# Performance work log

Hardware: AMD Instinct MI355X
Metric: run time of the kernel (lower is better)

Reference implementation:

```python
import jax, jax.numpy as jnp
import numpy as np

N = 16384; E = 131072; H = 128; RBF = 64; L = 4; NH = 8; HD = 16; SP = 100
CU = 10.0
ALPHA = 5.0 / CU
_start = float(np.exp(-CU))
MEANS = jnp.asarray(np.linspace(_start, 1.0, RBF, dtype=np.float32))
BETA = float(((2.0 / RBF) * (1.0 - _start)) ** -2)


def cutoff_fn(d):
    # cosine cutoff, cutoff_lower=0, cutoff_upper=CU
    return 0.5 * (jnp.cos(d * (np.pi / CU)) + 1.0) * (d < CU)


def expnorm_rbf(d):
    # d: (E,) -> (E, RBF)  exp-normal smearing (trainable=False)
    return cutoff_fn(d)[:, None] * jnp.exp(-BETA * (jnp.exp(-ALPHA * d)[:, None] - MEANS) ** 2)


def layernorm(x, g, b, eps=1e-6):
    m = x.mean(-1, keepdims=True)
    v = ((x - m) ** 2).mean(-1, keepdims=True)
    return (x - m) / jnp.sqrt(v + eps) * g + b


def setup_inputs() -> dict:
    key = jax.random.key(0)
    ks = jax.random.split(key, 20)
    def w(k, shape, fan):
        return jax.random.normal(k, shape, jnp.float32) / np.sqrt(fan)
    inp = {}
    inp["atomic_number"] = jax.random.randint(ks[0], (N,), 0, SP)
    inp["position"] = jax.random.normal(ks[1], (N, 3), jnp.float32) * 3.0
    inp["senders"] = jax.random.randint(ks[2], (E,), 0, N)
    inp["receivers"] = jax.random.randint(ks[3], (E,), 0, N)
    inp["embed1"] = w(ks[4], (SP, H), 1.0)
    inp["embed2"] = w(ks[5], (SP, H), 1.0)
    inp["nb_Wdist"] = w(ks[6], (RBF, H), RBF); inp["nb_bdist"] = jnp.zeros((H,), jnp.float32)
    inp["nb_Wcomb"] = w(ks[7], (2 * H, H), 2 * H); inp["nb_bcomb"] = jnp.zeros((H,), jnp.float32)
    inp["ln_g"] = jnp.ones((L, H), jnp.float32); inp["ln_b"] = jnp.zeros((L, H), jnp.float32)
    inp["Wq"] = w(ks[8], (L, H, H), H); inp["bq"] = jnp.zeros((L, H), jnp.float32)
    inp["Wk"] = w(ks[9], (L, H, H), H); inp["bk"] = jnp.zeros((L, H), jnp.float32)
    inp["Wv"] = w(ks[10], (L, H, 3 * H), H); inp["bv"] = jnp.zeros((L, 3 * H), jnp.float32)
    inp["Wvec"] = w(ks[11], (L, H, 3 * H), H)
    inp["Wdk"] = w(ks[12], (L, RBF, H), RBF); inp["bdk"] = jnp.zeros((L, H), jnp.float32)
    inp["Wdv"] = w(ks[13], (L, RBF, 3 * H), RBF); inp["bdv"] = jnp.zeros((L, 3 * H), jnp.float32)
    inp["Wo"] = w(ks[14], (L, H, 3 * H), H); inp["bo"] = jnp.zeros((L, 3 * H), jnp.float32)
    inp["coors_scale"] = jnp.full((L,), 0.01, jnp.float32)
    inp["lnf_g"] = jnp.ones((H,), jnp.float32); inp["lnf_b"] = jnp.zeros((H,), jnp.float32)
    return inp


def reference(atomic_number, position, senders, receivers, embed1, embed2,
              nb_Wdist, nb_bdist, nb_Wcomb, nb_bcomb, ln_g, ln_b,
              Wq, bq, Wk, bk, Wv, bv, Wvec, Wdk, bdk, Wdv, bdv, Wo, bo,
              coors_scale, lnf_g, lnf_b):
    eps = 1e-6
    n = atomic_number.shape[0]
    x = embed1[atomic_number]                               # (N,H)
    edge_vec = position[receivers] - position[senders]      # (E,3)
    edge_weight = jnp.linalg.norm(edge_vec + eps, axis=-1)  # (E,)
    edge_attr = expnorm_rbf(edge_weight)                    # (E,RBF)
    self_mask = senders == receivers
    mew = (edge_weight * (~self_mask) + self_mask)[:, None]
    mew = jnp.clip(mew, 0.01)                               # clip_during_norm
    edge_vec = edge_vec / mew                               # unit edge directions
    C = cutoff_fn(edge_weight[:, None])                     # (E,1)

    # Neighbor embedding
    Wmsg = (edge_attr @ nb_Wdist + nb_bdist) * C            # (E,H)
    msg = embed2[atomic_number[senders]] * Wmsg
    x_nb = jax.ops.segment_sum(msg, receivers, num_segments=n)
    x = jnp.concatenate([x, x_nb], axis=-1) @ nb_Wcomb + nb_bcomb

    vec = jnp.zeros((n, 3, H), x.dtype)
    for l in range(L):
        xn = layernorm(x, ln_g[l], ln_b[l])
        q = (xn @ Wq[l] + bq[l]).reshape(n, NH, HD)
        k = (xn @ Wk[l] + bk[l]).reshape(n, NH, HD)
        v = (xn @ Wv[l] + bv[l]).reshape(n, NH, 3 * HD)
        # qk_norm: l2-normalize per head
        q = q / (jnp.linalg.norm(q, axis=-1, keepdims=True) + eps)
        k = k / (jnp.linalg.norm(k, axis=-1, keepdims=True) + eps)
        # norm_coors (CoorsNorm with learned scale)
        vnorm = jnp.sqrt(jnp.clip((vec ** 2).sum(axis=1, keepdims=True), 1e-8))
        vn = vec / vnorm * coors_scale[l]
        vp = jnp.einsum('nvc,cd->nvd', vn, Wvec[l])          # (N,3,3H)
        vec1, vec2, vec3 = jnp.split(vp, 3, axis=-1)
        vec_dot = (vec1 * vec2).sum(axis=1)                  # (N,H)
        dk = jax.nn.silu(edge_attr @ Wdk[l] + bdk[l]).reshape(-1, NH, HD)
        dv = jax.nn.silu(edge_attr @ Wdv[l] + bdv[l]).reshape(-1, NH, 3 * HD)
        attn = (q[receivers] * k[senders] * dk).sum(-1)      # (E,NH)
        attn = jax.nn.silu(attn) * C                         # cutoff-weighted
        vj = v[senders] * dv                                 # (E,NH,3HD)
        xh, s1, s2 = jnp.split(vj, 3, axis=-1)
        xh = (xh * attn[..., None]).reshape(-1, H)
        s1 = s1.reshape(-1, H); s2 = s2.reshape(-1, H)
        vec_j = vec[senders] * s1[:, None, :] + s2[:, None, :] * edge_vec[:, :, None]
        x_agg = jax.ops.segment_sum(xh, receivers, num_segments=n)
        vec_agg = jax.ops.segment_sum(vec_j, receivers, num_segments=n)
        o = x_agg @ Wo[l] + bo[l]
        o1, o2, o3 = jnp.split(o, 3, axis=-1)
        x = x + vec_dot * o2 + o3
        vec = vec + vec3 * o1[:, None, :] + vec_agg
    x = layernorm(x, lnf_g, lnf_b)
    return (x, vec)
```

## Files before the change

### kernel.cpp

```cpp
#include <hip/hip_runtime.h>
#include <math.h>

#define NN 16384
#define NE 131072
#define HDIM 128
#define NRBF 64
#define NL 4

typedef __attribute__((ext_vector_type(8))) short short8;
typedef __attribute__((ext_vector_type(4))) float f32x4;
typedef __attribute__((ext_vector_type(2))) float f32x2;

__device__ __forceinline__ float siluf(float x){ return x / (1.0f + expf(-x)); }
__device__ __forceinline__ float cutofff(float d){
  return (d < 10.0f) ? 0.5f*(cosf(d*0.31415926535897932f)+1.0f) : 0.0f;
}
__device__ __forceinline__ unsigned short f2bf(float f){
  union{float f; unsigned u;} v; v.f = f;
  unsigned r = v.u + 0x7FFF + ((v.u>>16)&1);
  return (unsigned short)(r>>16);
}
__device__ __forceinline__ float bf2f(unsigned short b){
  union{unsigned u; float f;} v; v.u = ((unsigned)b)<<16;
  return v.f;
}
__device__ __forceinline__ float bflo(unsigned u){
  union{unsigned x; float f;} v; v.x = u<<16; return v.f;
}
__device__ __forceinline__ float bfhi(unsigned u){
  union{unsigned x; float f;} v; v.x = u & 0xffff0000u; return v.f;
}

__global__ void k_edge_geom(const float* __restrict__ pos, const int* __restrict__ snd,
                            const int* __restrict__ rcv, float* __restrict__ ew,
                            float* __restrict__ evec){
  int e = blockIdx.x*blockDim.x + threadIdx.x;
  if(e >= NE) return;
  int s = snd[e], r = rcv[e];
  float dx = pos[r*3+0]-pos[s*3+0];
  float dy = pos[r*3+1]-pos[s*3+1];
  float dz = pos[r*3+2]-pos[s*3+2];
  const float eps = 1e-6f;
  float d = sqrtf((dx+eps)*(dx+eps)+(dy+eps)*(dy+eps)+(dz+eps)*(dz+eps));
  ew[e] = d;
  float mew = (s==r) ? 1.0f : d;
  mew = fmaxf(mew, 0.01f);
  float inv = 1.0f/mew;
  evec[e*3+0]=dx*inv; evec[e*3+1]=dy*inv; evec[e*3+2]=dz*inv;
}

__global__ void k_hist(const int* __restrict__ rcv, int* __restrict__ deg){
  int e = blockIdx.x*256+threadIdx.x;
  if(e<NE) atomicAdd(&deg[rcv[e]],1);
}
__global__ __launch_bounds__(1024) void k_scan(const int* __restrict__ deg,
                                               int* __restrict__ off, int* __restrict__ cursor){
  __shared__ int part[1024];
  int t=threadIdx.x;
  int loc[16]; int s=0;
  #pragma unroll
  for(int i=0;i<16;i++){ loc[i]=s; s+=deg[t*16+i]; }
  part[t]=s; __syncthreads();
  for(int d=1;d<1024;d<<=1){
    int v=(t>=d)?part[t-d]:0; __syncthreads(); part[t]+=v; __syncthreads();
  }
  int excl = (t>0)?part[t-1]:0;
  #pragma unroll
  for(int i=0;i<16;i++){ int o=excl+loc[i]; off[t*16+i]=o; cursor[t*16+i]=o; }
  if(t==1023) off[NN]=part[1023];
}
__global__ void k_scatter(const int* __restrict__ rcv, int* __restrict__ cursor,
                          int* __restrict__ eidx){
  int e = blockIdx.x*256+threadIdx.x; if(e>=NE) return;
  int p = atomicAdd(&cursor[rcv[e]],1);
  eidx[p]=e;
}
__global__ void k_permute(const int* __restrict__ eidx, const float* __restrict__ ew,
                          const float* __restrict__ evec, const int* __restrict__ snd,
                          const int* __restrict__ rcv,
                          float* __restrict__ ews, float* __restrict__ cw,
                          float* __restrict__ evs, int* __restrict__ snds,
                          int* __restrict__ rcvs){
  int i = blockIdx.x*256+threadIdx.x; if(i>=NE) return;
  int e = eidx[i];
  float d = ew[e];
  ews[i]=d; cw[i]=cutofff(d);
  evs[i*3+0]=evec[e*3+0]; evs[i*3+1]=evec[e*3+1]; evs[i*3+2]=evec[e*3+2];
  snds[i]=snd[e]; rcvs[i]=rcv[e];
}

__global__ void k_cvt_nbT(const float* __restrict__ Wd, unsigned short* __restrict__ dst){
  int o = blockIdx.x*256+threadIdx.x; if(o>=HDIM*NRBF) return;
  int n=o>>6, k=o&63;
  dst[o] = f2bf(Wd[k*HDIM+n]);
}
__global__ void k_cvt_qkvT(const float* __restrict__ Wq, const float* __restrict__ Wk,
                           const float* __restrict__ Wv, unsigned short* __restrict__ dst){
  int o = blockIdx.x*256+threadIdx.x;
  if(o >= 4*640*128) return;
  int l = o/81920; int rem = o - l*81920;
  int n = rem>>7, k = rem&127;
  float v;
  if(n<128)      v = Wq[(size_t)l*16384 + k*128 + n];
  else if(n<256) v = Wk[(size_t)l*16384 + k*128 + (n-128)];
  else           v = Wv[(size_t)l*49152 + k*384 + (n-256)];
  dst[o]=f2bf(v);
}
__global__ void k_cvtT(const float* __restrict__ src, unsigned short* __restrict__ dst, int NC){
  int o = blockIdx.x*256+threadIdx.x;
  int tot = 4*NC*128; if(o>=tot) return;
  int l = o/(NC*128); int rem = o - l*NC*128;
  int n = rem>>7, k = rem&127;
  dst[o] = f2bf(src[(size_t)l*128*NC + k*NC + n]);
}
__global__ void k_wcvt4(const float* __restrict__ Wdk, const float* __restrict__ Wdv,
                        unsigned short* __restrict__ wbT4){
  int o = blockIdx.x*blockDim.x + threadIdx.x;
  if(o >= 4*512*64) return;
  int l = o >> 15; int rem = o & 32767;
  int n = rem >> 6, kk = rem & 63;
  float v = (n < 128) ? Wdk[(size_t)l*NRBF*HDIM + kk*HDIM + n]
                      : Wdv[(size_t)l*NRBF*384 + kk*384 + (n-128)];
  wbT4[o] = f2bf(v);
}
__global__ void k_bcvt4(const float* __restrict__ bdk, const float* __restrict__ bdv,
                        float* __restrict__ bias4){
  int o = threadIdx.x + blockIdx.x*blockDim.x;
  if(o >= 4*512) return;
  int l = o >> 9, c = o & 511;
  bias4[o] = (c < 128) ? bdk[l*HDIM + c] : bdv[l*384 + (c-128)];
}

__global__ __launch_bounds__(256) void k_nb_gemm(const float* __restrict__ ews,
    const float* __restrict__ cw, const int* __restrict__ snds,
    const int* __restrict__ z, const float* __restrict__ embed2,
    const unsigned short* __restrict__ nbT, const float* __restrict__ bd,
    unsigned short* __restrict__ msgc){
  __shared__ __align__(16) unsigned short Bl[HDIM*64];
  int t = threadIdx.x;
  int e0 = blockIdx.x*64;
  #pragma unroll
  for(int i=0;i<4;i++){
    int idx=i*256+t; int n=idx>>3, kc=idx&7;
    short8 val = *(const short8*)(nbT + n*64 + kc*8);
    *(short8*)((char*)Bl + n*128 + ((kc ^ (n&7))<<4)) = val;
  }
  int w=t>>6, l=t&63, lr=l&15, lg=l>>4;
  float d = ews[e0 + w*16 + lr];
  short8 a0, a1;
  {
    float edm = expf(-0.5f*d);
    float Cc = cutofff(d);
    const float start = expf(-10.0f);
    const float tmp = (2.0f/64.0f)*(1.0f-start);
    const float beta = 1.0f/(tmp*tmp);
    #pragma unroll
    for(int si=0;si<8;si++){
      float m0 = start + (1.0f-start)*((float)(lg*8+si)*(1.0f/63.0f));
      float m1 = start + (1.0f-start)*((float)(32+lg*8+si)*(1.0f/63.0f));
      float t0 = edm-m0, t1 = edm-m1;
      a0[si] = (short)f2bf(Cc*expf(-beta*t0*t0));
      a1[si] = (short)f2bf(Cc*expf(-beta*t1*t1));
    }
  }
  int sr[4]; float Cr[4]; int zz[4];
  #pragma unroll
  for(int r=0;r<4;r++){
    int i = e0 + w*16 + lg*4 + r;
    sr[r]=snds[i]; Cr[r]=cw[i]; zz[r]=z[sr[r]];
  }
  __syncthreads();
  #pragma unroll
  for(int nt=0;nt<8;nt++){
    int n=nt*16+lr;
    const char* bp=(const char*)Bl + n*128;
    short8 b0 = *(const short8*)(bp + (((lg  )^(n&7))<<4));
    short8 b1 = *(const short8*)(bp + (((4+lg)^(n&7))<<4));
    f32x4 acc={0.f,0.f,0.f,0.f};
    acc = __builtin_amdgcn_mfma_f32_16x16x32_bf16(a0,b0,acc,0,0,0);
    acc = __builtin_amdgcn_mfma_f32_16x16x32_bf16(a1,b1,acc,0,0,0);
    float bdn = bd[n];
    #pragma unroll
    for(int r=0;r<4;r++){
      float m = (acc[r]+bdn)*Cr[r]*embed2[(size_t)zz[r]*HDIM+n];
      msgc[(size_t)(e0+w*16+lg*4+r)*HDIM + n] = f2bf(m);
    }
  }
}
__global__ void k_nb_sweep(const int* __restrict__ off,
                           const unsigned short* __restrict__ msgc,
                           float* __restrict__ xnb){
  int j = threadIdx.x;
  int n0 = blockIdx.x*8;
  for(int nn=0;nn<8;nn++){
    int node=n0+nn;
    float acc=0.f;
    int ib=off[node], ie=off[node+1];
    for(int i=ib;i<ie;i++) acc += bf2f(msgc[(size_t)i*HDIM+j]);
    xnb[(size_t)node*HDIM+j]=acc;
  }
}

__global__ __launch_bounds__(256) void k_combine_b(
    const int* __restrict__ z, const float* __restrict__ embed1,
    const float* __restrict__ xnb, const float* __restrict__ Wc,
    const float* __restrict__ bc, float* __restrict__ x){
  __shared__ float sx[16][2*HDIM];
  int t = threadIdx.x; int n0 = blockIdx.x*16;
  #pragma unroll
  for(int i=0;i<16;i++){
    int idx = i*256+t; int nn = idx>>8, c = idx&255;
    int n = n0+nn;
    sx[nn][c] = (c<128) ? embed1[(size_t)z[n]*HDIM + c]
                        : xnb[(size_t)n*HDIM + (c-128)];
  }
  __syncthreads();
  int j = t&127, g = t>>7;
  float bcj = bc[j];
  float acc[8];
  #pragma unroll
  for(int r=0;r<8;r++) acc[r]=bcj;
  for(int i=0;i<2*HDIM;i++){
    float wv = Wc[i*HDIM+j];
    #pragma unroll
    for(int r=0;r<8;r++) acc[r] += sx[2*r+g][i]*wv;
  }
  #pragma unroll
  for(int r=0;r<8;r++) x[(size_t)(n0+2*r+g)*HDIM+j] = acc[r];
}

#define PADR 136
__global__ __launch_bounds__(256) void k_node_pre_m(
    const float* __restrict__ x, const float* __restrict__ vec,
    const float* __restrict__ lng, const float* __restrict__ lnb,
    const float* __restrict__ bq, const float* __restrict__ bk,
    const float* __restrict__ bv, const unsigned short* __restrict__ WqkvT,
    const unsigned short* __restrict__ WvecT, const float* __restrict__ cscale,
    unsigned short* __restrict__ qbf, unsigned short* __restrict__ kbf,
    unsigned short* __restrict__ vbf, float* __restrict__ vdot,
    float* __restrict__ vec3, int l){
  __shared__ unsigned short sxn[32][PADR];
  __shared__ unsigned short svn[3][32][PADR];
  int t = threadIdx.x, w = t>>6, lane = t&63;
  int n0 = blockIdx.x*32;
  float cs = cscale[l];
  float g0 = lng[l*HDIM+lane], g1 = lng[l*HDIM+64+lane];
  float be0 = lnb[l*HDIM+lane], be1 = lnb[l*HDIM+64+lane];
  for(int rr=0; rr<8; rr++){
    int nn = w*8+rr; int n = n0+nn;
    float x0 = x[(size_t)n*HDIM+lane], x1 = x[(size_t)n*HDIM+64+lane];
    float sum = x0+x1;
    #pragma unroll
    for(int m=1;m<=32;m<<=1) sum += __shfl_xor(sum,m);
    float mean = sum*(1.f/128.f);
    float d0 = x0-mean, d1 = x1-mean;
    float vs = d0*d0+d1*d1;
    #pragma unroll
    for(int m=1;m<=32;m<<=1) vs += __shfl_xor(vs,m);
    float rstd = rsqrtf(vs*(1.f/128.f)+1e-6f);
    sxn[nn][lane]    = f2bf(d0*rstd*g0 + be0);
    sxn[nn][64+lane] = f2bf(d1*rstd*g1 + be1);
    float va0 = vec[((size_t)n*3+0)*HDIM+lane], vb0 = vec[((size_t)n*3+0)*HDIM+64+lane];
    float va1 = vec[((size_t)n*3+1)*HDIM+lane], vb1 = vec[((size_t)n*3+1)*HDIM+64+lane];
    float va2 = vec[((size_t)n*3+2)*HDIM+lane], vb2 = vec[((size_t)n*3+2)*HDIM+64+lane];
    float iA = rsqrtf(fmaxf(va0*va0+va1*va1+va2*va2,1e-8f))*cs;
    float iB = rsqrtf(fmaxf(vb0*vb0+vb1*vb1+vb2*vb2,1e-8f))*cs;
    svn[0][nn][lane]=f2bf(va0*iA); svn[0][nn][64+lane]=f2bf(vb0*iB);
    svn[1][nn][lane]=f2bf(va1*iA); svn[1][nn][64+lane]=f2bf(vb1*iB);
    svn[2][nn][lane]=f2bf(va2*iA); svn[2][nn][64+lane]=f2bf(vb2*iB);
  }
  __syncthreads();
  int lr = lane&15, lg = lane>>4;
  int mt = w>>1, par = w&1;
  int rbase = mt*16;
  short8 a1[4];
  #pragma unroll
  for(int kk=0;kk<4;kk++) a1[kk] = *(const short8*)&sxn[rbase+lr][kk*32+lg*8];
  short8 a2[3][4];
  #pragma unroll
  for(int sp=0;sp<3;sp++)
    #pragma unroll
    for(int kk=0;kk<4;kk++) a2[sp][kk] = *(const short8*)&svn[sp][rbase+lr][kk*32+lg*8];

  const unsigned short* Bq = WqkvT + (size_t)l*640*128;
  for(int jj=0;jj<20;jj++){
    int j = jj*2+par;
    int col = j*16+lr;
    const unsigned short* bp = Bq + (size_t)col*128 + lg*8;
    f32x4 acc={0.f,0.f,0.f,0.f};
    #pragma unroll
    for(int kk=0;kk<4;kk++) acc = __builtin_amdgcn_mfma_f32_16x16x32_bf16(a1[kk], *(const short8*)(bp+kk*32), acc, 0,0,0);
    if(j < 16){
      float bias = (j<8) ? bq[l*HDIM+col] : bk[l*HDIM+col-128];
      float vv[4], s2[4];
      #pragma unroll
      for(int r=0;r<4;r++){ vv[r]=acc[r]+bias; s2[r]=vv[r]*vv[r]; }
      #pragma unroll
      for(int mm=1;mm<=8;mm<<=1){
        #pragma unroll
        for(int r=0;r<4;r++) s2[r] += __shfl_xor(s2[r],mm);
      }
      #pragma unroll
      for(int r=0;r<4;r++){
        int node = n0+rbase+lg*4+r;
        float vn_ = vv[r]/(sqrtf(s2[r])+1e-6f);
        if(j<8) qbf[(size_t)node*HDIM+col]     = f2bf(vn_);
        else    kbf[(size_t)node*HDIM+col-128] = f2bf(vn_);
      }
    } else {
      int c = col-256;
      float bias = bv[l*384+c];
      #pragma unroll
      for(int r=0;r<4;r++){
        int node = n0+rbase+lg*4+r;
        vbf[(size_t)node*384+c] = f2bf(acc[r]+bias);
      }
    }
  }
  const unsigned short* Bv = WvecT + (size_t)l*384*128;
  for(int jj=0;jj<4;jj++){
    int j = jj*2+par;
    int col = j*16+lr;
    short8 b1[4],b2[4],b3[4];
    #pragma unroll
    for(int kk=0;kk<4;kk++){
      b1[kk] = *(const short8*)(Bv + (size_t)(col    )*128 + kk*32+lg*8);
      b2[kk] = *(const short8*)(Bv + (size_t)(col+128)*128 + kk*32+lg*8);
      b3[kk] = *(const short8*)(Bv + (size_t)(col+256)*128 + kk*32+lg*8);
    }
    f32x4 vd={0.f,0.f,0.f,0.f};
    #pragma unroll
    for(int sp=0;sp<3;sp++){
      f32x4 p1={0.f,0.f,0.f,0.f}, p2={0.f,0.f,0.f,0.f}, p3={0.f,0.f,0.f,0.f};
      #pragma unroll
      for(int kk=0;kk<4;kk++){
        p1 = __builtin_amdgcn_mfma_f32_16x16x32_bf16(a2[sp][kk], b1[kk], p1, 0,0,0);
        p2 = __builtin_amdgcn_mfma_f32_16x16x32_bf16(a2[sp][kk], b2[kk], p2, 0,0,0);
        p3 = __builtin_amdgcn_mfma_f32_16x16x32_bf16(a2[sp][kk], b3[kk], p3, 0,0,0);
      }
      #pragma unroll
      for(int r=0;r<4;r++){
        vd[r] += p1[r]*p2[r];
        int node = n0+rbase+lg*4+r;
        vec3[((size_t)node*3+sp)*HDIM+col] = p3[r];
      }
    }
    #pragma unroll
    for(int r=0;r<4;r++){
      int node = n0+rbase+lg*4+r;
      vdot[(size_t)node*HDIM+col] = vd[r];
    }
  }
}

__global__ __launch_bounds__(256) void k_edge_fused2(
    const float* __restrict__ ews, const float* __restrict__ cw,
    const float* __restrict__ evs, const int* __restrict__ snds,
    const int* __restrict__ rcvs,
    const unsigned short* __restrict__ qbf, const unsigned short* __restrict__ kbf,
    const unsigned short* __restrict__ vbf, const unsigned short* __restrict__ vecbf,
    const unsigned short* __restrict__ wbT, const float* __restrict__ bias,
    float* __restrict__ xagg, float* __restrict__ vecagg){
  __shared__ __align__(16) unsigned short BD[512*64];
  __shared__ float sbias[512];
  __shared__ float scw[64];
  __shared__ float sev[64*3];
  __shared__ int   ssnd[64];
  __shared__ int   srcv[64];
  int t = threadIdx.x;
  int e0 = blockIdx.x*64;
  if(t < 64){ scw[t]=cw[e0+t]; ssnd[t]=snds[e0+t]; srcv[t]=rcvs[e0+t]; }
  if(t < 192) sev[t] = evs[e0*3 + t];
  sbias[t]=bias[t]; sbias[256+t]=bias[256+t];
  #pragma unroll
  for(int i=0;i<16;i++){
    int idx=i*256+t; int n=idx>>3, kc=idx&7;
    short8 val = *(const short8*)(wbT + n*64 + kc*8);
    *(short8*)((char*)BD + n*128 + ((kc ^ (n&7))<<4)) = val;
  }
  int w=t>>6, l=t&63, lr=l&15, lg=l>>4;
  float d = ews[e0 + w*16 + lr];
  short8 a0, a1;
  {
    float edm = expf(-0.5f*d);
    float Cc = cutofff(d);
    const float start = expf(-10.0f);
    const float tmp = (2.0f/64.0f)*(1.0f-start);
    const float beta = 1.0f/(tmp*tmp);
    #pragma unroll
    for(int si=0;si<8;si++){
      float m0 = start + (1.0f-start)*((float)(lg*8+si)*(1.0f/63.0f));
      float m1 = start + (1.0f-start)*((float)(32+lg*8+si)*(1.0f/63.0f));
      float t0 = edm-m0, t1 = edm-m1;
      a0[si] = (short)f2bf(Cc*expf(-beta*t0*t0));
      a1[si] = (short)f2bf(Cc*expf(-beta*t1*t1));
    }
  }
  __syncthreads();
  unsigned pk[64];
  #pragma unroll
  for(int nt=0;nt<32;nt++){
    int n=nt*16+lr;
    const char* bp=(const char*)BD + n*128;
    short8 b0 = *(const short8*)(bp + (((lg  )^(n&7))<<4));
    short8 b1 = *(const short8*)(bp + (((4+lg)^(n&7))<<4));
    f32x4 acc={0.f,0.f,0.f,0.f};
    acc = __builtin_amdgcn_mfma_f32_16x16x32_bf16(a0,b0,acc,0,0,0);
    acc = __builtin_amdgcn_mfma_f32_16x16x32_bf16(a1,b1,acc,0,0,0);
    float bs=sbias[n];
    pk[nt*2+0] = ((unsigned)f2bf(siluf(acc[1]+bs))<<16)|f2bf(siluf(acc[0]+bs));
    pk[nt*2+1] = ((unsigned)f2bf(siluf(acc[3]+bs))<<16)|f2bf(siluf(acc[2]+bs));
  }
  __syncthreads();
  #pragma unroll
  for(int nt=0;nt<32;nt++){
    int n=nt*16+lr;
    #pragma unroll
    for(int rr=0;rr<4;rr++){
      int el = w*16+lg*4+rr;
      unsigned short val = (unsigned short)(pk[nt*2+(rr>>1)]>>((rr&1)*16));
      *(unsigned short*)((char*)BD + el*1024 + ((n*2) ^ ((el&7)<<4))) = val;
    }
  }
  __syncthreads();
  {
    int j0 = 2*l;
    int hc0 = (l>>3)*48 + (j0&15);
    float ax0=0.f, ax1=0.f;
    float va00=0.f,va01=0.f, va10=0.f,va11=0.f, va20=0.f,va21=0.f;
    int cur = srcv[w*16];
    unsigned qd = *(const unsigned*)&qbf[(size_t)cur*HDIM + j0];
    int interior = 0;
    for(int e=0;e<16;e++){
      int el = w*16+e;
      int r = srcv[el];
      if(r != cur){
        if(interior){
          *(f32x2*)&xagg[(size_t)cur*HDIM+j0] = (f32x2){ax0,ax1};
          *(f32x2*)&vecagg[((size_t)cur*3+0)*HDIM+j0] = (f32x2){va00,va01};
          *(f32x2*)&vecagg[((size_t)cur*3+1)*HDIM+j0] = (f32x2){va10,va11};
          *(f32x2*)&vecagg[((size_t)cur*3+2)*HDIM+j0] = (f32x2){va20,va21};
        } else {
          atomicAdd(&xagg[(size_t)cur*HDIM+j0],ax0);
          atomicAdd(&xagg[(size_t)cur*HDIM+j0+1],ax1);
          atomicAdd(&vecagg[((size_t)cur*3+0)*HDIM+j0],va00);
          atomicAdd(&vecagg[((size_t)cur*3+0)*HDIM+j0+1],va01);
          atomicAdd(&vecagg[((size_t)cur*3+1)*HDIM+j0],va10);
          atomicAdd(&vecagg[((size_t)cur*3+1)*HDIM+j0+1],va11);
          atomicAdd(&vecagg[((size_t)cur*3+2)*HDIM+j0],va20);
          atomicAdd(&vecagg[((size_t)cur*3+2)*HDIM+j0+1],va21);
        }
        ax0=ax1=va00=va01=va10=va11=va20=va21=0.f;
        cur=r; interior=1;
        qd = *(const unsigned*)&qbf[(size_t)cur*HDIM + j0];
      }
      int s = ssnd[el];
      const char* dbase = (const char*)BD + el*1024;
      int sw_ = (el&7)<<4;
      unsigned kd  = *(const unsigned*)&kbf[(size_t)s*HDIM + j0];
      unsigned dkd = *(const unsigned*)(dbase + ((4*l)^sw_));
      float p = bflo(qd)*bflo(kd)*bflo(dkd) + bfhi(qd)*bfhi(kd)*bfhi(dkd);
      p += __shfl_xor(p,1); p += __shfl_xor(p,2); p += __shfl_xor(p,4);
      float attn = siluf(p)*scw[el];
      unsigned b0d = *(const unsigned*)(dbase + ((256+2*hc0)^sw_));
      unsigned b1d = *(const unsigned*)(dbase + ((288+2*hc0)^sw_));
      unsigned b2d = *(const unsigned*)(dbase + ((320+2*hc0)^sw_));
      const unsigned short* vs = vbf + (size_t)s*384;
      unsigned v0d = *(const unsigned*)&vs[hc0];
      unsigned v1d = *(const unsigned*)&vs[hc0+16];
      unsigned v2d = *(const unsigned*)&vs[hc0+32];
      ax0 += bflo(v0d)*bflo(b0d)*attn;
      ax1 += bfhi(v0d)*bfhi(b0d)*attn;
      float s10 = bflo(v1d)*bflo(b1d), s11 = bfhi(v1d)*bfhi(b1d);
      float s20 = bflo(v2d)*bflo(b2d), s21 = bfhi(v2d)*bfhi(b2d);
      float ev0=sev[el*3+0], ev1=sev[el*3+1], ev2=sev[el*3+2];
      unsigned w0 = *(const unsigned*)&vecbf[((size_t)s*3+0)*HDIM+j0];
      unsigned w1 = *(const unsigned*)&vecbf[((size_t)s*3+1)*HDIM+j0];
      unsigned w2 = *(const unsigned*)&vecbf[((size_t)s*3+2)*HDIM+j0];
      va00 += bflo(w0)*s10 + s20*ev0;  va01 += bfhi(w0)*s11 + s21*ev0;
      va10 += bflo(w1)*s10 + s20*ev1;  va11 += bfhi(w1)*s11 + s21*ev1;
      va20 += bflo(w2)*s10 + s20*ev2;  va21 += bfhi(w2)*s11 + s21*ev2;
    }
    atomicAdd(&xagg[(size_t)cur*HDIM+j0],ax0);
    atomicAdd(&xagg[(size_t)cur*HDIM+j0+1],ax1);
    atomicAdd(&vecagg[((size_t)cur*3+0)*HDIM+j0],va00);
    atomicAdd(&vecagg[((size_t)cur*3+0)*HDIM+j0+1],va01);
    atomicAdd(&vecagg[((size_t)cur*3+1)*HDIM+j0],va10);
    atomicAdd(&vecagg[((size_t)cur*3+1)*HDIM+j0+1],va11);
    atomicAdd(&vecagg[((size_t)cur*3+2)*HDIM+j0],va20);
    atomicAdd(&vecagg[((size_t)cur*3+2)*HDIM+j0+1],va21);
  }
}

__global__ __launch_bounds__(256) void k_node_update_m(
    const float* __restrict__ xagg, const float* __restrict__ vdot,
    const float* __restrict__ vec3, const float* __restrict__ vecagg,
    const unsigned short* __restrict__ WoT, const float* __restrict__ bo,
    float* __restrict__ x, float* __restrict__ vec,
    unsigned short* __restrict__ vecbf, int l){
  __shared__ unsigned short sxa[32][PADR];
  int t = threadIdx.x, w = t>>6, lane = t&63;
  int n0 = blockIdx.x*32;
  #pragma unroll
  for(int i=0;i<16;i++){
    int idx = i*256+t; int nn = idx>>7, j2 = idx&127;
    sxa[nn][j2] = f2bf(xagg[(size_t)(n0+nn)*HDIM + j2]);
  }
  __syncthreads();
  int lr = lane&15, lg = lane>>4;
  int mt = w>>1, par = w&1;
  int rbase = mt*16;
  short8 a[4];
  #pragma unroll
  for(int kk=0;kk<4;kk++)
    a[kk] = *(const short8*)&sxa[rbase+lr][kk*32+lg*8];
  const unsigned short* Bo = WoT + (size_t)l*384*128;
  for(int jj=0;jj<4;jj++){
    int j = jj*2+par;
    int col = j*16+lr;
    f32x4 ac1={0.f,0.f,0.f,0.f}, ac2={0.f,0.f,0.f,0.f}, ac3={0.f,0.f,0.f,0.f};
    #pragma unroll
    for(int kk=0;kk<4;kk++){
      ac1 = __builtin_amdgcn_mfma_f32_16x16x32_bf16(a[kk], *(const short8*)(Bo+(size_t)(col    )*128+kk*32+lg*8), ac1, 0,0,0);
      ac2 = __builtin_amdgcn_mfma_f32_16x16x32_bf16(a[kk], *(const short8*)(Bo+(size_t)(col+128)*128+kk*32+lg*8), ac2, 0,0,0);
      ac3 = __builtin_amdgcn_mfma_f32_16x16x32_bf16(a[kk], *(const short8*)(Bo+(size_t)(col+256)*128+kk*32+lg*8), ac3, 0,0,0);
    }
    float b1=bo[l*384+col], b2=bo[l*384+128+col], b3=bo[l*384+256+col];
    #pragma unroll
    for(int r=0;r<4;r++){
      int node = n0+rbase+lg*4+r;
      float o1=ac1[r]+b1, o2=ac2[r]+b2, o3=ac3[r]+b3;
      size_t xi = (size_t)node*HDIM+col;
      x[xi] += vdot[xi]*o2 + o3;
      #pragma unroll
      for(int sp=0;sp<3;sp++){
        size_t idx=((size_t)node*3+sp)*HDIM+col;
        float nv = vec[idx] + vec3[idx]*o1 + vecagg[idx];
        vec[idx]=nv; vecbf[idx]=f2bf(nv);
      }
    }
  }
}

__global__ void k_final(const float* __restrict__ x, const float* __restrict__ vec,
                        const float* __restrict__ g, const float* __restrict__ b,
                        float* __restrict__ out){
  int n=blockIdx.x; int t=threadIdx.x;
  float x0=x[(size_t)n*HDIM+t], x1=x[(size_t)n*HDIM+64+t];
  float sum=x0+x1;
  #pragma unroll
  for(int m=1;m<=32;m<<=1) sum += __shfl_xor(sum,m);
  float mean=sum*(1.f/128.f);
  float d0=x0-mean, d1=x1-mean;
  float vs=d0*d0+d1*d1;
  #pragma unroll
  for(int m=1;m<=32;m<<=1) vs += __shfl_xor(vs,m);
  float rstd=rsqrtf(vs*(1.f/128.f)+1e-6f);
  out[(size_t)n*HDIM+t]    = d0*rstd*g[t]+b[t];
  out[(size_t)n*HDIM+64+t] = d1*rstd*g[64+t]+b[64+t];
  float* ov = out + (size_t)NN*HDIM;
  for(int sp=0;sp<3;sp++){
    size_t idx=((size_t)n*3+sp)*HDIM;
    ov[idx+t]    = vec[idx+t];
    ov[idx+64+t] = vec[idx+64+t];
  }
}

extern "C" void kernel_launch(void* const* d_in, const int* in_sizes, int n_in,
                              void* d_out, int out_size, void* d_ws, size_t ws_size,
                              hipStream_t stream){
  const int*   z      = (const int*)  d_in[0];
  const float* pos    = (const float*)d_in[1];
  const int*   snd    = (const int*)  d_in[2];
  const int*   rcv    = (const int*)  d_in[3];
  const float* embed1 = (const float*)d_in[4];
  const float* embed2 = (const float*)d_in[5];
  const float* nbWd   = (const float*)d_in[6];
  const float* nbbd   = (const float*)d_in[7];
  const float* nbWc   = (const float*)d_in[8];
  const float* nbbc   = (const float*)d_in[9];
  const float* lng    = (const float*)d_in[10];
  const float* lnb    = (const float*)d_in[11];
  const float* Wq     = (const float*)d_in[12];
  const float* bq     = (const float*)d_in[13];
  const float* Wk     = (const float*)d_in[14];
  const float* bk     = (const float*)d_in[15];
  const float* Wv     = (const float*)d_in[16];
  const float* bv     = (const float*)d_in[17];
  const float* Wvec   = (const float*)d_in[18];
  const float* Wdk    = (const float*)d_in[19];
  const float* bdk    = (const float*)d_in[20];
  const float* Wdv    = (const float*)d_in[21];
  const float* bdv    = (const float*)d_in[22];
  const float* Wo     = (const float*)d_in[23];
  const float* bo     = (const float*)d_in[24];
  const float* cscale = (const float*)d_in[25];
  const float* lnfg   = (const float*)d_in[26];
  const float* lnfb   = (const float*)d_in[27];
  float* out = (float*)d_out;

  float* ws = (float*)d_ws;
  unsigned short* region = (unsigned short*)ws;  ws += (size_t)NE*HDIM/2;
  float* ew   = (float*)region;
  float* evec = ew + NE;
  unsigned short* msgc = region;

  float* ews   = ws;  ws += NE;
  float* cw    = ws;  ws += NE;
  float* evs   = ws;  ws += 3*NE;
  float* x     = ws;  ws += (size_t)NN*HDIM;
  float* vdot  = ws;  ws += (size_t)NN*HDIM;
  float* xagg  = ws;  ws += (size_t)NN*HDIM;
  float* vec3  = ws;  ws += (size_t)NN*384;
  float* vecagg= ws;  ws += (size_t)NN*384;
  float* vec   = ws;  ws += (size_t)NN*384;
  float* bias4 = ws;  ws += 4*512;
  int* deg    = (int*)ws; ws += NN;
  int* off    = (int*)ws; ws += NN+8;
  int* cursor = (int*)ws; ws += NN;
  int* eidx   = (int*)ws; ws += NE;
  int* snds   = (int*)ws; ws += NE;
  int* rcvs   = (int*)ws; ws += NE;
  unsigned short* qbf   = (unsigned short*)ws;
  unsigned short* kbf   = qbf  + (size_t)NN*HDIM;
  unsigned short* vbf   = kbf  + (size_t)NN*HDIM;
  unsigned short* vecbf = vbf  + (size_t)NN*384;
  unsigned short* WqkvT = vecbf+ (size_t)NN*384;
  unsigned short* WvecT = WqkvT + (size_t)4*640*128;
  unsigned short* WoT   = WvecT + (size_t)4*384*128;
  unsigned short* nbT   = WoT   + (size_t)4*384*128;
  unsigned short* wbT4  = nbT   + (size_t)HDIM*NRBF;

  float* xnb = vdot;

  k_edge_geom<<<(NE+255)/256,256,0,stream>>>(pos,snd,rcv,ew,evec);
  hipMemsetAsync(deg,0,NN*4,stream);
  k_hist<<<NE/256,256,0,stream>>>(rcv,deg);
  k_scan<<<1,1024,0,stream>>>(deg,off,cursor);
  k_scatter<<<NE/256,256,0,stream>>>(rcv,cursor,eidx);
  k_permute<<<NE/256,256,0,stream>>>(eidx,ew,evec,snd,rcv,ews,cw,evs,snds,rcvs);
  k_cvt_nbT<<<(HDIM*NRBF)/256,256,0,stream>>>(nbWd,nbT);
  k_nb_gemm<<<NE/64,256,0,stream>>>(ews,cw,snds,z,embed2,nbT,nbbd,msgc);
  k_nb_sweep<<<NN/8,128,0,stream>>>(off,msgc,xnb);
  k_combine_b<<<NN/16,256,0,stream>>>(z,embed1,xnb,nbWc,nbbc,x);
  hipMemsetAsync(vec,0,(size_t)NN*384*4,stream);
  hipMemsetAsync(vecbf,0,(size_t)NN*384*2,stream);
  k_cvt_qkvT<<<(4*640*128)/256,256,0,stream>>>(Wq,Wk,Wv,WqkvT);
  k_cvtT<<<(4*384*128)/256,256,0,stream>>>(Wvec,WvecT,384);
  k_cvtT<<<(4*384*128)/256,256,0,stream>>>(Wo,WoT,384);
  k_wcvt4<<<(4*512*64)/256,256,0,stream>>>(Wdk,Wdv,wbT4);
  k_bcvt4<<<8,256,0,stream>>>(bdk,bdv,bias4);
  for(int l=0;l<NL;l++){
    k_node_pre_m<<<NN/32,256,0,stream>>>(x,vec,lng,lnb,bq,bk,bv,WqkvT,WvecT,cscale,
                                         qbf,kbf,vbf,vdot,vec3,l);
    hipMemsetAsync(xagg,0,(size_t)NN*HDIM*4,stream);
    hipMemsetAsync(vecagg,0,(size_t)NN*384*4,stream);
    k_edge_fused2<<<NE/64,256,0,stream>>>(ews,cw,evs,snds,rcvs,qbf,kbf,vbf,vecbf,
                                          wbT4 + (size_t)l*512*64, bias4 + l*512,
                                          xagg,vecagg);
    k_node_update_m<<<NN/32,256,0,stream>>>(xagg,vdot,vec3,vecagg,WoT,bo,x,vec,vecbf,l);
  }
  k_final<<<NN,64,0,stream>>>(x,vec,lnfg,lnfb,out);
}
```

Measured before the change: 929.3 us.

## Halve edge tile to 32 edges per block and stage weights in two halves

Each edge block now handles 32 edges instead of 64. The 512x64 dk/dv weight matrix is staged through shared memory in two 256-column halves, and the 4 waves are split into 2 row-tiles by 2 column-chunks. This cuts LDS from about 64KB to about 32KB and the per-thread pk register array from 64 to 32 entries, which should raise occupancy. In exchange the launch has twice as many blocks, so the weight matrix is reloaded from global memory twice as often, there are extra barriers, and each wave's receiver-run segments shrink to 8 edges, which can mean more atomics at segment boundaries.

Result: faster. 898.1 us, median of 3 (-3.4%).

```diff
diff --git a/kernel.cpp b/kernel.cpp
--- a/kernel.cpp
+++ b/kernel.cpp
@@ -353,7 +353,7 @@
   }
 }
 
-__global__ __launch_bounds__(256) void k_edge_fused2(
+__global__ __launch_bounds__(256) void k_edge_fused3(
     const float* __restrict__ ews, const float* __restrict__ cw,
     const float* __restrict__ evs, const int* __restrict__ snds,
     const int* __restrict__ rcvs,
@@ -361,25 +361,22 @@
     const unsigned short* __restrict__ vbf, const unsigned short* __restrict__ vecbf,
     const unsigned short* __restrict__ wbT, const float* __restrict__ bias,
     float* __restrict__ xagg, float* __restrict__ vecagg){
-  __shared__ __align__(16) unsigned short BD[512*64];
+  __shared__ __align__(16) unsigned short R[256*64];
   __shared__ float sbias[512];
-  __shared__ float scw[64];
-  __shared__ float sev[64*3];
-  __shared__ int   ssnd[64];
-  __shared__ int   srcv[64];
+  __shared__ float scw[32];
+  __shared__ float sev[96];
+  __shared__ int   ssnd[32];
+  __shared__ int   srcv[32];
   int t = threadIdx.x;
-  int e0 = blockIdx.x*64;
-  if(t < 64){ scw[t]=cw[e0+t]; ssnd[t]=snds[e0+t]; srcv[t]=rcvs[e0+t]; }
-  if(t < 192) sev[t] = evs[e0*3 + t];
+  int e0 = blockIdx.x*32;
+  if(t < 32){ scw[t]=cw[e0+t]; ssnd[t]=snds[e0+t]; srcv[t]=rcvs[e0+t]; }
+  if(t < 96) sev[t] = evs[e0*3 + t];
   sbias[t]=bias[t]; sbias[256+t]=bias[256+t];
-  #pragma unroll
-  for(int i=0;i<16;i++){
-    int idx=i*256+t; int n=idx>>3, kc=idx&7;
-    short8 val = *(const short8*)(wbT + n*64 + kc*8);
-    *(short8*)((char*)BD + n*128 + ((kc ^ (n&7))<<4)) = val;
-  }
+
   int w=t>>6, l=t&63, lr=l&15, lg=l>>4;
-  float d = ews[e0 + w*16 + lr];
+  int rt = w&1, ch = w>>1;
+  int row = rt*16 + lr;
+  float d = ews[e0 + row];
   short8 a0, a1;
   {
     float edm = expf(-0.5f*d);
@@ -396,30 +393,43 @@
       a1[si] = (short)f2bf(Cc*expf(-beta*t1*t1));
     }
   }
+  unsigned pk[32];
+  #pragma unroll
+  for(int h=0; h<2; h++){
+    __syncthreads();
+    #pragma unroll
+    for(int i=0;i<8;i++){
+      int idx = i*256+t; int nl = idx>>3, kc = idx&7;
+      short8 val = *(const short8*)(wbT + (size_t)(h*256+nl)*64 + kc*8);
+      *(short8*)((char*)R + nl*128 + ((kc ^ (nl&7))<<4)) = val;
+    }
+    __syncthreads();
+    #pragma unroll
+    for(int nt=0;nt<8;nt++){
+      int nl = ch*128 + nt*16 + lr;
+      const char* bp=(const char*)R + nl*128;
+      short8 b0 = *(const short8*)(bp + (((lg  )^(nl&7))<<4));
+      short8 b1 = *(const short8*)(bp + (((4+lg)^(nl&7))<<4));
+      f32x4 acc={0.f,0.f,0.f,0.f};
+      acc = __builtin_amdgcn_mfma_f32_16x16x32_bf16(a0,b0,acc,0,0,0);
+      acc = __builtin_amdgcn_mfma_f32_16x16x32_bf16(a1,b1,acc,0,0,0);
+      float bs=sbias[h*256+nl];
+      pk[(h*8+nt)*2+0] = ((unsigned)f2bf(siluf(acc[1]+bs))<<16)|f2bf(siluf(acc[0]+bs));
+      pk[(h*8+nt)*2+1] = ((unsigned)f2bf(siluf(acc[3]+bs))<<16)|f2bf(siluf(acc[2]+bs));
+    }
+  }
   __syncthreads();
-  unsigned pk[64];
-  #pragma unroll
-  for(int nt=0;nt<32;nt++){
-    int n=nt*16+lr;
-    const char* bp=(const char*)BD + n*128;
-    short8 b0 = *(const short8*)(bp + (((lg  )^(n&7))<<4));
-    short8 b1 = *(const short8*)(bp + (((4+lg)^(n&7))<<4));
-    f32x4 acc={0.f,0.f,0.f,0.f};
-    acc = __builtin_amdgcn_mfma_f32_16x16x32_bf16(a0,b0,acc,0,0,0);
-    acc = __builtin_amdgcn_mfma_f32_16x16x32_bf16(a1,b1,acc,0,0,0);
-    float bs=sbias[n];
-    pk[nt*2+0] = ((unsigned)f2bf(siluf(acc[1]+bs))<<16)|f2bf(siluf(acc[0]+bs));
-    pk[nt*2+1] = ((unsigned)f2bf(siluf(acc[3]+bs))<<16)|f2bf(siluf(acc[2]+bs));
-  }
-  __syncthreads();
-  #pragma unroll
-  for(int nt=0;nt<32;nt++){
-    int n=nt*16+lr;
-    #pragma unroll
-    for(int rr=0;rr<4;rr++){
-      int el = w*16+lg*4+rr;
-      unsigned short val = (unsigned short)(pk[nt*2+(rr>>1)]>>((rr&1)*16));
-      *(unsigned short*)((char*)BD + el*1024 + ((n*2) ^ ((el&7)<<4))) = val;
+  #pragma unroll
+  for(int h=0;h<2;h++){
+    #pragma unroll
+    for(int nt=0;nt<8;nt++){
+      int n = h*256 + ch*128 + nt*16 + lr;
+      #pragma unroll
+      for(int rr=0;rr<4;rr++){
+        int el = rt*16+lg*4+rr;
+        unsigned short val = (unsigned short)(pk[(h*8+nt)*2+(rr>>1)]>>((rr&1)*16));
+        *(unsigned short*)((char*)R + el*1024 + ((n*2) ^ ((el&7)<<4))) = val;
+      }
     }
   }
   __syncthreads();
@@ -428,11 +438,11 @@
     int hc0 = (l>>3)*48 + (j0&15);
     float ax0=0.f, ax1=0.f;
     float va00=0.f,va01=0.f, va10=0.f,va11=0.f, va20=0.f,va21=0.f;
-    int cur = srcv[w*16];
+    int cur = srcv[w*8];
     unsigned qd = *(const unsigned*)&qbf[(size_t)cur*HDIM + j0];
     int interior = 0;
-    for(int e=0;e<16;e++){
-      int el = w*16+e;
+    for(int e=0;e<8;e++){
+      int el = w*8+e;
       int r = srcv[el];
       if(r != cur){
         if(interior){
@@ -455,7 +465,7 @@
         qd = *(const unsigned*)&qbf[(size_t)cur*HDIM + j0];
       }
       int s = ssnd[el];
-      const char* dbase = (const char*)BD + el*1024;
+      const char* dbase = (const char*)R + el*1024;
       int sw_ = (el&7)<<4;
       unsigned kd  = *(const unsigned*)&kbf[(size_t)s*HDIM + j0];
       unsigned dkd = *(const unsigned*)(dbase + ((4*l)^sw_));
@@ -655,7 +665,7 @@
                                          qbf,kbf,vbf,vdot,vec3,l);
     hipMemsetAsync(xagg,0,(size_t)NN*HDIM*4,stream);
     hipMemsetAsync(vecagg,0,(size_t)NN*384*4,stream);
-    k_edge_fused2<<<NE/64,256,0,stream>>>(ews,cw,evs,snds,rcvs,qbf,kbf,vbf,vecbf,
+    k_edge_fused3<<<NE/32,256,0,stream>>>(ews,cw,evs,snds,rcvs,qbf,kbf,vbf,vecbf,
                                           wbT4 + (size_t)l*512*64, bias4 + l*512,
                                           xagg,vecagg);
     k_node_update_m<<<NN/32,256,0,stream>>>(xagg,vdot,vec3,vecagg,WoT,bo,x,vec,vecbf,l);
```
